# Optimization experiments

Measured on AMD Instinct MI355X. Metric: run time of the kernel, lower is better.

The kernel has to match this reference:

```python
import jax, jax.numpy as jnp
import numpy as np

V_TH = 1.0
V_RESET = 0.0
ALPHA = 4.0  # sigmoid surrogate sharpness used by the Triton backward kernel


@jax.custom_vjp
def spike_fn(over_th):
    # Heaviside forward; sigmoid surrogate gradient in backward.
    return (over_th >= 0).astype(over_th.dtype)


def _spike_fwd(over_th):
    return spike_fn(over_th), over_th


def _spike_bwd(over_th, g):
    sig = jax.nn.sigmoid(ALPHA * over_th)
    return (g * (1.0 - sig) * sig * ALPHA,)


spike_fn.defvjp(_spike_fwd, _spike_bwd)


def setup_inputs() -> dict:
    key = jax.random.key(0)
    k1, _ = jax.random.split(key)
    T, B, D = 32, 128, 8192
    x_seq = jax.random.normal(k1, (T, B, D), dtype=jnp.float32)
    v_init = jnp.zeros((B, D), dtype=jnp.float32)  # module init: v = v_reset = 0.0
    return {"x_seq": x_seq, "v_init": v_init}


def reference(x_seq, v_init):
    # IF neuron, multi-step, hard reset:
    #   h_t   = x_t + v_{t-1}
    #   s_t   = H(h_t - v_th)
    #   v_t   = h_t * (1 - s_t) + v_reset * s_t
    def step(v, x):
        h = x + v
        s = spike_fn(h - V_TH)
        v_next = h * (1.0 - s) + V_RESET * s
        return v_next, s

    _, spike_seq = jax.lax.scan(step, v_init, x_seq)
    return spike_seq
```

## Files before the change

kernel.cpp:

```cpp
#include <hip/hip_runtime.h>


template <int T>
__global__ __launch_bounds__(256) void if_node_vec4_fixed(
    const float* __restrict__ x,
    const float* __restrict__ v0,
    float* __restrict__ out,
    long n4)
{
    long i = (long)blockIdx.x * blockDim.x + threadIdx.x;
    if (i >= n4) return;

    const float4* x4  = (const float4*)x;
    const float4* v04 = (const float4*)v0;
    float4*       o4  = (float4*)out;

    float4 v = v04[i];

#pragma unroll
    for (int t = 0; t < T; ++t) {
        float4 xv = x4[(long)t * n4 + i];
        float hx = xv.x + v.x;
        float hy = xv.y + v.y;
        float hz = xv.z + v.z;
        float hw = xv.w + v.w;
        bool sx = (hx - 1.0f) >= 0.0f;
        bool sy = (hy - 1.0f) >= 0.0f;
        bool sz = (hz - 1.0f) >= 0.0f;
        bool sw = (hw - 1.0f) >= 0.0f;
        float4 s;
        s.x = sx ? 1.0f : 0.0f;
        s.y = sy ? 1.0f : 0.0f;
        s.z = sz ? 1.0f : 0.0f;
        s.w = sw ? 1.0f : 0.0f;
        v.x = sx ? 0.0f : hx;
        v.y = sy ? 0.0f : hy;
        v.z = sz ? 0.0f : hz;
        v.w = sw ? 0.0f : hw;
        o4[(long)t * n4 + i] = s;
    }
}

__global__ __launch_bounds__(256) void if_node_vec4_generic(
    const float* __restrict__ x, const float* __restrict__ v0,
    float* __restrict__ out, long n4, int T)
{
    long i = (long)blockIdx.x * blockDim.x + threadIdx.x;
    if (i >= n4) return;
    const float4* x4  = (const float4*)x;
    const float4* v04 = (const float4*)v0;
    float4*       o4  = (float4*)out;
    float4 v = v04[i];
    for (int t = 0; t < T; ++t) {
        float4 xv = x4[(long)t * n4 + i];
        float hx = xv.x + v.x;
        float hy = xv.y + v.y;
        float hz = xv.z + v.z;
        float hw = xv.w + v.w;
        bool sx = (hx - 1.0f) >= 0.0f;
        bool sy = (hy - 1.0f) >= 0.0f;
        bool sz = (hz - 1.0f) >= 0.0f;
        bool sw = (hw - 1.0f) >= 0.0f;
        float4 s;
        s.x = sx ? 1.0f : 0.0f;
        s.y = sy ? 1.0f : 0.0f;
        s.z = sz ? 1.0f : 0.0f;
        s.w = sw ? 1.0f : 0.0f;
        v.x = sx ? 0.0f : hx;
        v.y = sy ? 0.0f : hy;
        v.z = sz ? 0.0f : hz;
        v.w = sw ? 0.0f : hw;
        o4[(long)t * n4 + i] = s;
    }
}

__global__ __launch_bounds__(256) void if_node_scalar(
    const float* __restrict__ x, const float* __restrict__ v0,
    float* __restrict__ out, long n, int T)
{
    long i = (long)blockIdx.x * blockDim.x + threadIdx.x;
    if (i >= n) return;
    float v = v0[i];
    for (int t = 0; t < T; ++t) {
        float h = x[(long)t * n + i] + v;
        bool s = (h - 1.0f) >= 0.0f;
        out[(long)t * n + i] = s ? 1.0f : 0.0f;
        v = s ? 0.0f : h;
    }
}

extern "C" void kernel_launch(void* const* d_in, const int* in_sizes, int n_in,
                              void* d_out, int out_size, void* d_ws, size_t ws_size,
                              hipStream_t stream) {
    const float* x  = (const float*)d_in[0];
    const float* v0 = (const float*)d_in[1];
    float* out = (float*)d_out;

    long n = in_sizes[1];
    int  T = (int)(in_sizes[0] / n);

    if ((n & 3) == 0) {
        long n4 = n >> 2;
        int block = 256;
        long grid = (n4 + block - 1) / block;
        if (T == 32) {
            if_node_vec4_fixed<32><<<dim3((unsigned)grid), dim3(block), 0, stream>>>(
                x, v0, out, n4);
        } else {
            if_node_vec4_generic<<<dim3((unsigned)grid), dim3(block), 0, stream>>>(
                x, v0, out, n4, T);
        }
    } else {
        int block = 256;
        long grid = (n + block - 1) / block;
        if_node_scalar<<<dim3((unsigned)grid), dim3(block), 0, stream>>>(
            x, v0, out, n, T);
    }
}
```

Baseline: 243.0 us.

## Switch to float2 lanes with grouped software-prefetched loads and nontemporal stores

Each thread now handles two floats instead of four, which doubles the grid, and processes the time sequence in groups of eight steps. The next group's loads are issued before the current group is computed, so more memory requests stay in flight. Output stores use nontemporal hints so the write-once spike data bypasses cache retention. The trade-offs are narrower 8-byte accesses per request and higher register use from the prefetch buffers.

```diff
diff --git a/kernel.cpp b/kernel.cpp
--- a/kernel.cpp
+++ b/kernel.cpp
@@ -1,76 +1,80 @@
 #include <hip/hip_runtime.h>
 
 
-template <int T>
-__global__ __launch_bounds__(256) void if_node_vec4_fixed(
+typedef float v2f __attribute__((ext_vector_type(2)));
+
+template <int T, int KB>
+__global__ __launch_bounds__(256) void if_node_f2_pipe(
     const float* __restrict__ x,
     const float* __restrict__ v0,
     float* __restrict__ out,
-    long n4)
+    long n2)
 {
     long i = (long)blockIdx.x * blockDim.x + threadIdx.x;
-    if (i >= n4) return;
+    if (i >= n2) return;
 
-    const float4* x4  = (const float4*)x;
-    const float4* v04 = (const float4*)v0;
-    float4*       o4  = (float4*)out;
+    const v2f* __restrict__ x2 = (const v2f*)x;
+    v2f*       __restrict__ o2 = (v2f*)out;
 
-    float4 v = v04[i];
+    v2f v = ((const v2f*)v0)[i];
+
+    constexpr int G = T / KB;
+    v2f cur[KB];
+    v2f nxt[KB];
 
 #pragma unroll
-    for (int t = 0; t < T; ++t) {
-        float4 xv = x4[(long)t * n4 + i];
-        float hx = xv.x + v.x;
-        float hy = xv.y + v.y;
-        float hz = xv.z + v.z;
-        float hw = xv.w + v.w;
-        bool sx = (hx - 1.0f) >= 0.0f;
-        bool sy = (hy - 1.0f) >= 0.0f;
-        bool sz = (hz - 1.0f) >= 0.0f;
-        bool sw = (hw - 1.0f) >= 0.0f;
-        float4 s;
-        s.x = sx ? 1.0f : 0.0f;
-        s.y = sy ? 1.0f : 0.0f;
-        s.z = sz ? 1.0f : 0.0f;
-        s.w = sw ? 1.0f : 0.0f;
-        v.x = sx ? 0.0f : hx;
-        v.y = sy ? 0.0f : hy;
-        v.z = sz ? 0.0f : hz;
-        v.w = sw ? 0.0f : hw;
-        o4[(long)t * n4 + i] = s;
+    for (int k = 0; k < KB; ++k)
+        cur[k] = x2[(long)k * n2 + i];
+
+#pragma unroll
+    for (int g = 0; g < G; ++g) {
+        if (g + 1 < G) {
+#pragma unroll
+            for (int k = 0; k < KB; ++k)
+                nxt[k] = x2[(long)((g + 1) * KB + k) * n2 + i];
+        }
+#pragma unroll
+        for (int k = 0; k < KB; ++k) {
+            float hx = cur[k].x + v.x;
+            float hy = cur[k].y + v.y;
+            bool sx = (hx - 1.0f) >= 0.0f;
+            bool sy = (hy - 1.0f) >= 0.0f;
+            v2f s;
+            s.x = sx ? 1.0f : 0.0f;
+            s.y = sy ? 1.0f : 0.0f;
+            v.x = sx ? 0.0f : hx;
+            v.y = sy ? 0.0f : hy;
+            __builtin_nontemporal_store(s, &o2[(long)(g * KB + k) * n2 + i]);
+        }
+        if (g + 1 < G) {
+#pragma unroll
+            for (int k = 0; k < KB; ++k)
+                cur[k] = nxt[k];
+        }
     }
 }
 
-__global__ __launch_bounds__(256) void if_node_vec4_generic(
+__global__ __launch_bounds__(256) void if_node_f2_generic(
     const float* __restrict__ x, const float* __restrict__ v0,
-    float* __restrict__ out, long n4, int T)
+    float* __restrict__ out, long n2, int T)
 {
     long i = (long)blockIdx.x * blockDim.x + threadIdx.x;
-    if (i >= n4) return;
-    const float4* x4  = (const float4*)x;
-    const float4* v04 = (const float4*)v0;
-    float4*       o4  = (float4*)out;
-    float4 v = v04[i];
+    if (i >= n2) return;
+    const v2f* x2 = (const v2f*)x;
+    v2f*       o2 = (v2f*)out;
+    v2f v = ((const v2f*)v0)[i];
     for (int t = 0; t < T; ++t) {
-        float4 xv = x4[(long)t * n4 + i];
+        v2f xv = x2[(long)t * n2 + i];
         float hx = xv.x + v.x;
         float hy = xv.y + v.y;
-        float hz = xv.z + v.z;
-        float hw = xv.w + v.w;
         bool sx = (hx - 1.0f) >= 0.0f;
         bool sy = (hy - 1.0f) >= 0.0f;
-        bool sz = (hz - 1.0f) >= 0.0f;
-        bool sw = (hw - 1.0f) >= 0.0f;
-        float4 s;
+        v2f s;
         s.x = sx ? 1.0f : 0.0f;
         s.y = sy ? 1.0f : 0.0f;
-        s.z = sz ? 1.0f : 0.0f;
-        s.w = sw ? 1.0f : 0.0f;
         v.x = sx ? 0.0f : hx;
         v.y = sy ? 0.0f : hy;
-        v.z = sz ? 0.0f : hz;
-        v.w = sw ? 0.0f : hw;
-        o4[(long)t * n4 + i] = s;
+        o2[(long)t * n2 + i] = s;
     }
 }
 
@@ -99,19 +103,18 @@
     long n = in_sizes[1];
     int  T = (int)(in_sizes[0] / n);
 
-    if ((n & 3) == 0) {
-        long n4 = n >> 2;
-        int block = 256;
-        long grid = (n4 + block - 1) / block;
-        if (T == 32) {
-            if_node_vec4_fixed<32><<<dim3((unsigned)grid), dim3(block), 0, stream>>>(
-                x, v0, out, n4);
-        } else {
-            if_node_vec4_generic<<<dim3((unsigned)grid), dim3(block), 0, stream>>>(
-                x, v0, out, n4, T);
-        }
+    int block = 256;
+    if (T == 32 && (n & 1) == 0) {
+        long n2 = n >> 1;
+        long grid = (n2 + block - 1) / block;
+        if_node_f2_pipe<32, 8><<<dim3((unsigned)grid), dim3(block), 0, stream>>>(
+            x, v0, out, n2);
+    } else if ((n & 1) == 0) {
+        long n2 = n >> 1;
+        long grid = (n2 + block - 1) / block;
+        if_node_f2_generic<<<dim3((unsigned)grid), dim3(block), 0, stream>>>(
+            x, v0, out, n2, T);
     } else {
-        int block = 256;
         long grid = (n + block - 1) / block;
         if_node_scalar<<<dim3((unsigned)grid), dim3(block), 0, stream>>>(
             x, v0, out, n, T);
```

New measurement: 237.6 us. -2.2%, faster.
